# Optimization experiments

Measured on AMD Instinct MI355X. Metric: run time of the kernel, lower is better.

## Reference

```python
import jax, jax.numpy as jnp
import numpy as np

B, N_ORB, N_F, HID = 32768, 256, 64, 128


def setup_inputs() -> dict:
    key = jax.random.key(0)
    k1, k2, k3 = jax.random.split(key, 3)
    # Occupation-number configurations: exactly N_F ones per row (fermion number conservation).
    scores = jax.random.uniform(k1, (B, N_ORB))
    occ_idx = jnp.argsort(scores, axis=-1)[:, :N_F]  # (B, N_F) random occupied orbitals
    n = jnp.zeros((B, N_ORB), jnp.float32).at[jnp.arange(B)[:, None], occ_idx].set(1.0)
    # Slater orbital matrix M: (n_orbitals, n_fermions)
    M = jax.random.normal(k2, (N_ORB, N_F), jnp.float32) * 0.3 + jnp.eye(N_ORB, N_F, dtype=jnp.float32)
    # Jastrow linear layer (lecun_normal-style init, zero bias — flax defaults)
    W = jax.random.normal(k3, (N_ORB, HID), jnp.float32) * (1.0 / np.sqrt(N_ORB))
    b = jnp.zeros((HID,), jnp.float32)
    return {"n": n, "M": M, "W": W, "b": b}


def reference(n, M, W, b):
    # Jastrow factor: sum(tanh(Linear(n)))  -> (B,)
    J = jnp.tanh(n @ W + b).sum(axis=-1)
    # Occupied-orbital indices, ascending (matches n.nonzero(size=n_fermions)).
    n_f = M.shape[1]
    idx = jnp.sort(jnp.argsort(-n, axis=-1)[:, :n_f], axis=-1)  # (B, n_f)
    # Gather occupied rows of M -> small Slater matrices (B, n_f, n_f)
    A = M[idx]
    sign, logabsdet = jnp.linalg.slogdet(A)
    # complex log-determinant: log|det| + log(sign)
    log_slater = logabsdet.astype(jnp.complex64) + jnp.log(sign.astype(jnp.complex64))
    return log_slater + J.astype(jnp.complex64)
```

## Files before the change

### kernel.cpp

```cpp
#include <hip/hip_runtime.h>

#define N_ORB 256
#define N_F   64
#define HID   128

__device__ __forceinline__ float readlane_f(float x, int l) {
    return __int_as_float(__builtin_amdgcn_readlane(__float_as_int(x), l));
}

__device__ __forceinline__ unsigned wave_max_u32(unsigned v) {
    unsigned t;
    t = (unsigned)__builtin_amdgcn_update_dpp((int)v, (int)v, 0x111, 0xF, 0xF, false); v = v > t ? v : t;
    t = (unsigned)__builtin_amdgcn_update_dpp((int)v, (int)v, 0x112, 0xF, 0xF, false); v = v > t ? v : t;
    t = (unsigned)__builtin_amdgcn_update_dpp((int)v, (int)v, 0x114, 0xF, 0xF, false); v = v > t ? v : t;
    t = (unsigned)__builtin_amdgcn_update_dpp((int)v, (int)v, 0x118, 0xF, 0xF, false); v = v > t ? v : t;
    t = (unsigned)__builtin_amdgcn_update_dpp((int)v, (int)v, 0x142, 0xF, 0xF, false); v = v > t ? v : t;
    t = (unsigned)__builtin_amdgcn_update_dpp((int)v, (int)v, 0x143, 0xF, 0xF, false); v = v > t ? v : t;
    return v;
}

__global__ __launch_bounds__(256)
__attribute__((amdgpu_waves_per_eu(6, 7)))
void njs_kernel(
    const float* __restrict__ nmat,
    const float* __restrict__ M,
    const float* __restrict__ W,
    const float* __restrict__ bvec,
    float* __restrict__ out,
    int write_complex)
{
    const int lane = threadIdx.x & 63;
    const int wid  = threadIdx.x >> 6;
    const int row  = blockIdx.x * 4 + wid;
    __shared__ int idx_lds[4][N_F];

    const float4 nv = *reinterpret_cast<const float4*>(nmat + (size_t)row * N_ORB + lane * 4);
    unsigned bits = (nv.x > 0.5f ? 1u : 0u) | (nv.y > 0.5f ? 2u : 0u) |
                    (nv.z > 0.5f ? 4u : 0u) | (nv.w > 0.5f ? 8u : 0u);
    unsigned long long bal0 = __ballot(bits & 1u);
    unsigned long long bal1 = __ballot(bits & 2u);
    unsigned long long bal2 = __ballot(bits & 4u);
    unsigned long long bal3 = __ballot(bits & 8u);
    const unsigned long long below = (1ull << lane) - 1ull;
    int r = __popcll(bal0 & below) + __popcll(bal1 & below) +
            __popcll(bal2 & below) + __popcll(bal3 & below);
    #pragma unroll
    for (int c = 0; c < 4; ++c) {
        if (bits & (1u << c)) {
            idx_lds[wid][r] = lane * 4 + c;
            ++r;
        }
    }
    __syncthreads();
    const int o = idx_lds[wid][lane];

    float a[N_F];
    {
        const float* Mr = M + (size_t)o * N_F;
        #pragma unroll
        for (int j = 0; j < N_F; j += 4) {
            const float4 v = *reinterpret_cast<const float4*>(Mr + j);
            a[j] = v.x; a[j+1] = v.y; a[j+2] = v.z; a[j+3] = v.w;
        }
    }

    unsigned long long used = 0ull;
    int   expsum = 0;
    float vprod  = 1.0f;
    int   neg    = 0;

    #pragma unroll
    for (int k = 0; k < N_F; ++k) {
        const unsigned mykey = (((unsigned)__float_as_int(fabsf(a[k]))) & ~63u) | (unsigned)lane;
        const unsigned key   = ((used >> lane) & 1ull) ? 0u : mykey;
        const unsigned kmax  = wave_max_u32(key);
        const int ps   = __builtin_amdgcn_readlane((int)kmax, 63) & 63;
        const int ipiv = __builtin_amdgcn_readlane(__float_as_int(a[k]), ps);

        expsum += (ipiv >> 23) & 0xFF;
        neg    ^= (int)(((unsigned)ipiv) >> 31);
        vprod  *= __int_as_float((ipiv & 0x7FFFFF) | 0x3F800000);

        const unsigned long long belowp = (1ull << ps) - 1ull;
        neg ^= (int)((__popcll(used) - __popcll(used & belowp)) & 1);
        used |= (1ull << ps);

        const float piv = __int_as_float(ipiv);
        float rp = __builtin_amdgcn_rcpf(piv);
        rp = rp * fmaf(-piv, rp, 2.0f);
        const float mult = a[k] * rp;
        #pragma unroll
        for (int j = k + 1; j < N_F; ++j) {
            a[j] = fmaf(-mult, readlane_f(a[j], ps), a[j]);
        }
    }
    const float ld2 = (float)(expsum - 64 * 127) + __log2f(vprod);

    float y0 = 0.0f, y1 = 0.0f;
    #pragma unroll
    for (int i = 0; i < N_F; ++i) {
        const int os = __builtin_amdgcn_readlane(o, i);
        const float2 w = *reinterpret_cast<const float2*>(W + (size_t)os * HID + lane * 2);
        y0 += w.x; y1 += w.y;
    }
    y0 += bvec[lane * 2];
    y1 += bvec[lane * 2 + 1];
    float t = tanhf(y0) + tanhf(y1);
    #pragma unroll
    for (int d = 32; d >= 1; d >>= 1) t += __shfl_xor(t, d);

    if (lane == 0) {
        const float real = ld2 * 0.6931471805599453f + t;
        if (write_complex) {
            out[(size_t)row * 2]     = real;
            out[(size_t)row * 2 + 1] = (neg & 1) ? 3.14159265358979323846f : 0.0f;
        } else {
            out[row] = real;
        }
    }
}

extern "C" void kernel_launch(void* const* d_in, const int* in_sizes, int n_in,
                              void* d_out, int out_size, void* d_ws, size_t ws_size,
                              hipStream_t stream) {
    const float* nmat = (const float*)d_in[0];
    const float* M    = (const float*)d_in[1];
    const float* W    = (const float*)d_in[2];
    const float* b    = (const float*)d_in[3];
    float* out = (float*)d_out;
    const int B = in_sizes[0] / N_ORB;
    const int write_complex = (out_size >= 2 * B) ? 1 : 0;
    njs_kernel<<<B / 4, 256, 0, stream>>>(nmat, M, W, b, out, write_complex);
}
```

Baseline: 474.0 us.

## Offload first 16 Slater columns to LDS to cut register pressure

Keeps the first 16 columns of each per-row Slater matrix in padded LDS and eliminates them with a rolled loop that reads the pivot row from LDS. The remaining 48 columns stay in registers with the readlane broadcast. The goal is fewer VGPRs so the occupancy hint can rise to 8 waves per EU, at the cost of LDS traffic and rolled loops in the first phase. The W gather loop is also only partly unrolled.

```diff
diff --git a/kernel.cpp b/kernel.cpp
--- a/kernel.cpp
+++ b/kernel.cpp
@@ -3,6 +3,8 @@
 #define N_ORB 256
 #define N_F   64
 #define HID   128
+#define NLDS  16
+#define LP    17
 
 __device__ __forceinline__ float readlane_f(float x, int l) {
     return __int_as_float(__builtin_amdgcn_readlane(__float_as_int(x), l));
@@ -20,7 +22,7 @@
 }
 
 __global__ __launch_bounds__(256)
-__attribute__((amdgpu_waves_per_eu(6, 7)))
+__attribute__((amdgpu_waves_per_eu(6, 8)))
 void njs_kernel(
     const float* __restrict__ nmat,
     const float* __restrict__ M,
@@ -32,7 +34,9 @@
     const int lane = threadIdx.x & 63;
     const int wid  = threadIdx.x >> 6;
     const int row  = blockIdx.x * 4 + wid;
-    __shared__ int idx_lds[4][N_F];
+
+    __shared__ int   idx_lds[4][N_F];
+    __shared__ float Acol[4][N_F * LP];
 
     const float4 nv = *reinterpret_cast<const float4*>(nmat + (size_t)row * N_ORB + lane * 4);
     unsigned bits = (nv.x > 0.5f ? 1u : 0u) | (nv.y > 0.5f ? 2u : 0u) |
@@ -54,33 +58,37 @@
     __syncthreads();
     const int o = idx_lds[wid][lane];
 
-    float a[N_F];
-    {
-        const float* Mr = M + (size_t)o * N_F;
-        #pragma unroll
-        for (int j = 0; j < N_F; j += 4) {
-            const float4 v = *reinterpret_cast<const float4*>(Mr + j);
-            a[j] = v.x; a[j+1] = v.y; a[j+2] = v.z; a[j+3] = v.w;
-        }
+    float a[N_F - NLDS];
+    const float* Mr = M + (size_t)o * N_F;
+    float* Al = &Acol[wid][lane * LP];
+    #pragma unroll
+    for (int j = 0; j < NLDS; j += 4) {
+        const float4 v = *reinterpret_cast<const float4*>(Mr + j);
+        Al[j] = v.x; Al[j+1] = v.y; Al[j+2] = v.z; Al[j+3] = v.w;
     }
+    #pragma unroll
+    for (int s = 0; s < N_F - NLDS; s += 4) {
+        const float4 v = *reinterpret_cast<const float4*>(Mr + NLDS + s);
+        a[s] = v.x; a[s+1] = v.y; a[s+2] = v.z; a[s+3] = v.w;
+    }
+    asm volatile("s_waitcnt lgkmcnt(0)" ::: "memory");
 
     unsigned long long used = 0ull;
     int   expsum = 0;
     float vprod  = 1.0f;
     int   neg    = 0;
 
-    #pragma unroll
-    for (int k = 0; k < N_F; ++k) {
-        const unsigned mykey = (((unsigned)__float_as_int(fabsf(a[k]))) & ~63u) | (unsigned)lane;
+    #pragma unroll 1
+    for (int k = 0; k < NLDS; ++k) {
+        const float myAk = Al[k];
+        const unsigned mykey = (((unsigned)__float_as_int(fabsf(myAk))) & ~63u) | (unsigned)lane;
         const unsigned key   = ((used >> lane) & 1ull) ? 0u : mykey;
-        const unsigned kmax  = wave_max_u32(key);
-        const int ps   = __builtin_amdgcn_readlane((int)kmax, 63) & 63;
-        const int ipiv = __builtin_amdgcn_readlane(__float_as_int(a[k]), ps);
+        const int ps   = __builtin_amdgcn_readlane((int)wave_max_u32(key), 63) & 63;
+        const int ipiv = __builtin_amdgcn_readlane(__float_as_int(myAk), ps);
 
         expsum += (ipiv >> 23) & 0xFF;
         neg    ^= (int)(((unsigned)ipiv) >> 31);
         vprod  *= __int_as_float((ipiv & 0x7FFFFF) | 0x3F800000);
-
         const unsigned long long belowp = (1ull << ps) - 1ull;
         neg ^= (int)((__popcll(used) - __popcll(used & belowp)) & 1);
         used |= (1ull << ps);
@@ -88,16 +96,46 @@
         const float piv = __int_as_float(ipiv);
         float rp = __builtin_amdgcn_rcpf(piv);
         rp = rp * fmaf(-piv, rp, 2.0f);
-        const float mult = a[k] * rp;
+        const float mult = myAk * rp;
+
+        const float* Ap = &Acol[wid][ps * LP];
+        #pragma unroll 1
+        for (int j = k + 1; j < NLDS; ++j)
+            Al[j] = fmaf(-mult, Ap[j], Al[j]);
         #pragma unroll
-        for (int j = k + 1; j < N_F; ++j) {
-            a[j] = fmaf(-mult, readlane_f(a[j], ps), a[j]);
-        }
+        for (int s = 0; s < N_F - NLDS; ++s)
+            a[s] = fmaf(-mult, readlane_f(a[s], ps), a[s]);
+    }
+
+    #pragma unroll
+    for (int k = NLDS; k < N_F; ++k) {
+        const int   s0  = k - NLDS;
+        const float cur = a[s0];
+        const unsigned mykey = (((unsigned)__float_as_int(fabsf(cur))) & ~63u) | (unsigned)lane;
+        const unsigned key   = ((used >> lane) & 1ull) ? 0u : mykey;
+        const int ps   = __builtin_amdgcn_readlane((int)wave_max_u32(key), 63) & 63;
+        const int ipiv = __builtin_amdgcn_readlane(__float_as_int(cur), ps);
+
+        expsum += (ipiv >> 23) & 0xFF;
+        neg    ^= (int)(((unsigned)ipiv) >> 31);
+        vprod  *= __int_as_float((ipiv & 0x7FFFFF) | 0x3F800000);
+        const unsigned long long belowp = (1ull << ps) - 1ull;
+        neg ^= (int)((__popcll(used) - __popcll(used & belowp)) & 1);
+        used |= (1ull << ps);
+
+        const float piv = __int_as_float(ipiv);
+        float rp = __builtin_amdgcn_rcpf(piv);
+        rp = rp * fmaf(-piv, rp, 2.0f);
+        const float mult = cur * rp;
+
+        #pragma unroll
+        for (int s = s0 + 1; s < N_F - NLDS; ++s)
+            a[s] = fmaf(-mult, readlane_f(a[s], ps), a[s]);
     }
     const float ld2 = (float)(expsum - 64 * 127) + __log2f(vprod);
 
     float y0 = 0.0f, y1 = 0.0f;
-    #pragma unroll
+    #pragma unroll 8
     for (int i = 0; i < N_F; ++i) {
         const int os = __builtin_amdgcn_readlane(o, i);
         const float2 w = *reinterpret_cast<const float2*>(W + (size_t)os * HID + lane * 2);
```

After: 443.8 us. 1.07x faster.
